# Kernel optimization log

Measured on AMD Instinct MI355X. Metric: run time of the kernel, lower is better.

The kernel has to match this reference:

```python
import jax, jax.numpy as jnp
import numpy as np

N_NODES = 100000
N_EDGES = 1600000
DIMS = [2, 16, 32, 32, 32, 32, 32, 16, 2]


def setup_inputs() -> dict:
    key = jax.random.key(0)
    ks = jax.random.split(key, 20)
    inp = {}
    inp["x"] = jax.random.normal(ks[0], (N_NODES, DIMS[0]), dtype=jnp.float32)
    inp["edge_index"] = jax.random.randint(ks[1], (2, N_EDGES), 0, N_NODES, dtype=jnp.int64)
    for i in range(8):
        fan_in, fan_out = DIMS[i], DIMS[i + 1]
        scale = 1.0 / np.sqrt(fan_in)
        inp[f"W{i+1}"] = jax.random.uniform(ks[2 + i], (fan_in, fan_out), minval=-scale, maxval=scale, dtype=jnp.float32)
        inp[f"b{i+1}"] = jnp.zeros((fan_out,), dtype=jnp.float32)
    return inp


def _gcn_layer(h, W, b, src, dst, norm, n):
    # GCNConv: h' = D^{-1/2} (A+I) D^{-1/2} (h W) + b
    m = (h @ W)[src] * norm[:, None]          # [E+N, d_out] gathered messages
    return jax.ops.segment_sum(m, dst, num_segments=n) + b


def reference(x, edge_index, W1, b1, W2, b2, W3, b3, W4, b4, W5, b5, W6, b6, W7, b7, W8, b8):
    n = x.shape[0]
    x_orig = x[:, :2]
    loops = jnp.arange(n, dtype=edge_index.dtype)
    src = jnp.concatenate([edge_index[0], loops])  # self-loops appended
    dst = jnp.concatenate([edge_index[1], loops])
    deg = jax.ops.segment_sum(jnp.ones(src.shape[0], x.dtype), dst, num_segments=n)
    dinv = jnp.where(deg > 0, jax.lax.rsqrt(deg), 0.0)
    norm = dinv[src] * dinv[dst]               # symmetric normalization per edge
    params = [(W1, b1), (W2, b2), (W3, b3), (W4, b4), (W5, b5), (W6, b6), (W7, b7), (W8, b8)]
    h = x
    for i, (W, b) in enumerate(params):
        h = _gcn_layer(h, W, b, src, dst, norm, n)
        if i < 7:
            h = jax.nn.relu(h)  # dropout is identity in eval mode
    return h + x_orig
```

## Files before the change

kernel.cpp:

```cpp
#include <hip/hip_runtime.h>
#include <hip/hip_fp16.h>

#define NN 100000
#define NE 1600000
#define SCAN_BLK 1024
#define NBLK ((NN + SCAN_BLK - 1) / SCAN_BLK)

#define EB 6144
#define NBE ((NE + EB - 1) / EB)
#define BSH 10
#define NBUCK ((NN + 1023) >> BSH)
#define BCAP 18432


__global__ void k_init(int* __restrict__ bcur) {
    int i = blockIdx.x * blockDim.x + threadIdx.x;
    if (i < NBUCK) bcur[i] = i * BCAP;
}

__global__ __launch_bounds__(256) void k_bucket(
    const int* __restrict__ ei, int* __restrict__ bcur,
    long long* __restrict__ pairs, int nE) {
    __shared__ int cnt[NBUCK];
    __shared__ int sc[NBUCK];
    __shared__ int rc[NBUCK];
    __shared__ int gbase[NBUCK];
    __shared__ int tmp[256];
    __shared__ long long st[EB];

    int base = blockIdx.x * EB;
    int lim = nE - base; if (lim > EB) lim = EB;
    int tid = threadIdx.x;

    for (int i = tid; i < NBUCK; i += 256) cnt[i] = 0;
    __syncthreads();
    for (int i = tid; i < lim; i += 256) {
        int d = ei[nE + base + i];
        atomicAdd(&cnt[d >> BSH], 1);
    }
    __syncthreads();
    {
        int v = (tid < NBUCK) ? cnt[tid] : 0;
        tmp[tid] = v;
        __syncthreads();
        for (int off = 1; off < 256; off <<= 1) {
            int add = (tid >= off) ? tmp[tid - off] : 0;
            __syncthreads();
            tmp[tid] += add;
            __syncthreads();
        }
        if (tid < NBUCK) {
            int e = tmp[tid] - v;
            sc[tid] = e;
            rc[tid] = e;
            gbase[tid] = (v > 0) ? atomicAdd(&bcur[tid], v) : 0;
        }
    }
    __syncthreads();
    for (int i = tid; i < lim; i += 256) {
        int s = ei[base + i];
        int d = ei[nE + base + i];
        int p = atomicAdd(&rc[d >> BSH], 1);
        st[p] = ((long long)d << 32) | (unsigned int)s;
    }
    __syncthreads();
    for (int i = tid; i < lim; i += 256) {
        long long pr = st[i];
        int b = (int)(pr >> 32) >> BSH;
        pairs[gbase[b] + (i - sc[b])] = pr;
    }
}

__global__ __launch_bounds__(256) void k_count2(
    const long long* __restrict__ pairs, const int* __restrict__ bcur,
    int* __restrict__ deg) {
    __shared__ int cnt[1 << BSH];
    int b = blockIdx.x;
    int gb = b * BCAP;
    int m = bcur[b] - gb;
    for (int i = threadIdx.x; i < (1 << BSH); i += 256) cnt[i] = 0;
    __syncthreads();
    for (int i = threadIdx.x; i < m; i += 256) {
        int d = (int)(pairs[gb + i] >> 32);
        atomicAdd(&cnt[d & ((1 << BSH) - 1)], 1);
    }
    __syncthreads();
    int base = b << BSH;
    for (int i = threadIdx.x; i < (1 << BSH); i += 256) {
        int v = base + i;
        if (v < NN) deg[v] = cnt[i];
    }
}

__global__ __launch_bounds__(SCAN_BLK) void k_scan1(
    const int* __restrict__ deg, int* __restrict__ exc, int* __restrict__ bsum, int n) {
    __shared__ int sh[SCAN_BLK];
    int tid = threadIdx.x;
    int i = blockIdx.x * SCAN_BLK + tid;
    int v = (i < n) ? ((deg[i] + 7) & ~7) : 0;
    sh[tid] = v;
    __syncthreads();
    for (int off = 1; off < SCAN_BLK; off <<= 1) {
        int add = (tid >= off) ? sh[tid - off] : 0;
        __syncthreads();
        sh[tid] += add;
        __syncthreads();
    }
    if (i < n) exc[i] = sh[tid] - v;
    if (tid == SCAN_BLK - 1) bsum[blockIdx.x] = sh[tid];
}

__global__ __launch_bounds__(128) void k_scan2(int* __restrict__ bsum, int nb) {
    __shared__ int sh[128];
    int tid = threadIdx.x;
    int v = (tid < nb) ? bsum[tid] : 0;
    sh[tid] = v;
    __syncthreads();
    for (int off = 1; off < 128; off <<= 1) {
        int add = (tid >= off) ? sh[tid - off] : 0;
        __syncthreads();
        sh[tid] += add;
        __syncthreads();
    }
    if (tid < nb) bsum[tid] = sh[tid] - v;
}

__global__ __launch_bounds__(SCAN_BLK) void k_scan3(
    const int* __restrict__ exc, const int* __restrict__ bsum,
    const int* __restrict__ deg, const float* __restrict__ x,
    int* __restrict__ rowptr, float* __restrict__ dinv,
    __half2* __restrict__ hd0, int n) {
    int i = blockIdx.x * SCAN_BLK + threadIdx.x;
    if (i >= n) return;
    int r = exc[i] + bsum[blockIdx.x];
    rowptr[i] = r;
    float dv = rsqrtf((float)(deg[i] + 1));
    dinv[i] = dv;
    hd0[i] = __floats2half2_rn(x[2 * i] * dv, x[2 * i + 1] * dv);
    if (i == n - 1) rowptr[n] = r + ((deg[i] + 7) & ~7);
    if (i == 0) hd0[n] = __floats2half2_rn(0.f, 0.f);
}

__global__ __launch_bounds__(256) void k_fill3(
    const long long* __restrict__ pairs, const int* __restrict__ bcur,
    const int* __restrict__ rowptr, int* __restrict__ csr_src) {
    __shared__ int lcur[1 << BSH];
    int b = blockIdx.x;
    int gb = b * BCAP;
    int m = bcur[b] - gb;
    int base = b << BSH;
    for (int i = threadIdx.x; i < (1 << BSH); i += 256) {
        int v = base + i;
        lcur[i] = (v < NN) ? rowptr[v] : 0;
    }
    __syncthreads();
    for (int i = threadIdx.x; i < m; i += 256) {
        long long pr = pairs[gb + i];
        int d = (int)(pr >> 32);
        int s = (int)(pr & 0xffffffffLL);
        int pos = atomicAdd(&lcur[d & ((1 << BSH) - 1)], 1);
        csr_src[pos] = s;
    }
    __syncthreads();
    for (int i = threadIdx.x; i < (1 << BSH); i += 256) {
        int v = base + i;
        if (v < NN) {
            int e = lcur[i];
            int pe = rowptr[v + 1];
            for (; e < pe; ++e) csr_src[e] = NN;
        }
    }
}


__global__ __launch_bounds__(256) void k_layer1(
    const int* __restrict__ rowptr, const int* __restrict__ csr_src,
    const __half2* __restrict__ hd0, const float* __restrict__ Wg,
    const float* __restrict__ bg, const float* __restrict__ dinv,
    __half* __restrict__ hd1, int n) {
    __shared__ float sW[32];
    if (threadIdx.x < 32) sW[threadIdx.x] = Wg[threadIdx.x];
    __syncthreads();
    int v = blockIdx.x * 16 + threadIdx.x / 16;
    int l = threadIdx.x & 15;
    if (v > n) return;
    if (v == n) { hd1[v * 16 + l] = __float2half(0.f); return; }
    int lo = rowptr[v], hi = rowptr[v + 1];
    float a0 = 0.f, a1 = 0.f;
    for (int j = lo + l; j < hi; j += 16) {
        float2 h = __half22float2(hd0[csr_src[j]]);
        a0 += h.x; a1 += h.y;
    }
#pragma unroll
    for (int off = 8; off >= 1; off >>= 1) {
        a0 += __shfl_xor(a0, off, 16);
        a1 += __shfl_xor(a1, off, 16);
    }
    float dv = dinv[v];
    float2 hs = __half22float2(hd0[v]);
    a0 = (a0 + hs.x) * dv;
    a1 = (a1 + hs.y) * dv;
    float o = bg[l] + a0 * sW[l] + a1 * sW[16 + l];
    hd1[v * 16 + l] = __float2half(fmaxf(o, 0.f) * dv);
}

template <int DIN, int DOUT, bool RELU, bool LAST>
__global__ __launch_bounds__(256) void k_layerU(
    const int* __restrict__ rowptr, const int* __restrict__ csr_src,
    const __half* __restrict__ hd_in, const float* __restrict__ Wg,
    const float* __restrict__ bg, const float* __restrict__ dinv,
    const float* __restrict__ xorig, __half* __restrict__ hout_h,
    float* __restrict__ hout_f, int n) {
    constexpr int PQ = DIN / 2;
    int lane = threadIdx.x & 63;

    int v = blockIdx.x * 4 + (threadIdx.x >> 6);
    if (v > n) return;
    if (v == n) {
        if (!LAST && lane < DOUT) hout_h[(size_t)v * DOUT + lane] = __float2half(0.f);
        return;
    }
    int q = lane & (PQ - 1);
    int lo = rowptr[v], hi = rowptr[v + 1];
    int nch = (hi - lo) >> 3;
    const uint* hp = (const uint*)hd_in;
    float accx = 0.f, accy = 0.f;

    if constexpr (DIN == 32) {
        int el = lane >> 4;
        int b0 = lo + el;
        int sA0 = csr_src[b0 +  0], sB0 = csr_src[b0 +  4];
        int sA1 = csr_src[b0 +  8], sB1 = csr_src[b0 + 12];
        int sA2 = csr_src[b0 + 16], sB2 = csr_src[b0 + 20];
        int sA3 = csr_src[b0 + 24], sB3 = csr_src[b0 + 28];
        if (nch < 1) { sA0 = NN; sB0 = NN; }
        if (nch < 2) { sA1 = NN; sB1 = NN; }
        if (nch < 3) { sA2 = NN; sB2 = NN; }
        if (nch < 4) { sA3 = NN; sB3 = NN; }
        uint uA0 = hp[(size_t)sA0 * 16 + q], uB0 = hp[(size_t)sB0 * 16 + q];
        uint uA1 = hp[(size_t)sA1 * 16 + q], uB1 = hp[(size_t)sB1 * 16 + q];
        uint uA2 = hp[(size_t)sA2 * 16 + q], uB2 = hp[(size_t)sB2 * 16 + q];
        uint uA3 = hp[(size_t)sA3 * 16 + q], uB3 = hp[(size_t)sB3 * 16 + q];
        __half2 h0 = __hadd2(*(const __half2*)&uA0, *(const __half2*)&uB0);
        __half2 h1 = __hadd2(*(const __half2*)&uA1, *(const __half2*)&uB1);
        __half2 h2 = __hadd2(*(const __half2*)&uA2, *(const __half2*)&uB2);
        __half2 h3 = __hadd2(*(const __half2*)&uA3, *(const __half2*)&uB3);
        float2 f0 = __half22float2(h0), f1 = __half22float2(h1);
        float2 f2 = __half22float2(h2), f3 = __half22float2(h3);
        accx = (f0.x + f1.x) + (f2.x + f3.x);
        accy = (f0.y + f1.y) + (f2.y + f3.y);
        for (int j = lo + 32; j < hi; j += 8) {
            int sA = csr_src[j + el], sB = csr_src[j + 4 + el];
            uint uA = hp[(size_t)sA * 16 + q], uB = hp[(size_t)sB * 16 + q];
            __half2 hs = __hadd2(*(const __half2*)&uA, *(const __half2*)&uB);
            float2 f = __half22float2(hs);
            accx += f.x; accy += f.y;
        }
    } else {
        int el = lane >> 3;
        int b0 = lo + el;
        int s0 = csr_src[b0 +  0];
        int s1 = csr_src[b0 +  8];
        int s2 = csr_src[b0 + 16];
        int s3 = csr_src[b0 + 24];
        if (nch < 1) s0 = NN;
        if (nch < 2) s1 = NN;
        if (nch < 3) s2 = NN;
        if (nch < 4) s3 = NN;
        uint u0 = hp[(size_t)s0 * 8 + q];
        uint u1 = hp[(size_t)s1 * 8 + q];
        uint u2 = hp[(size_t)s2 * 8 + q];
        uint u3 = hp[(size_t)s3 * 8 + q];
        __half2 ha = __hadd2(*(const __half2*)&u0, *(const __half2*)&u1);
        __half2 hb = __hadd2(*(const __half2*)&u2, *(const __half2*)&u3);
        float2 fa = __half22float2(ha), fb = __half22float2(hb);
        accx = fa.x + fb.x;
        accy = fa.y + fb.y;
        for (int j = lo + 32; j < hi; j += 8) {
            int s = csr_src[j + el];
            uint u = hp[(size_t)s * 8 + q];
            float2 f = __half22float2(*(const __half2*)&u);
            accx += f.x; accy += f.y;
        }
    }
#pragma unroll
    for (int off = PQ; off < 64; off <<= 1) {
        accx += __shfl_xor(accx, off, 64);
        accy += __shfl_xor(accy, off, 64);
    }
    {
        uint us = hp[(size_t)v * PQ + q];
        float2 fs = __half22float2(*(const __half2*)&us);
        accx += fs.x; accy += fs.y;
    }
    float dv = dinv[v];
    float a0 = accx * dv;
    float a1 = accy * dv;

    if constexpr (DIN == 32) {
        int el2 = lane >> 4;
        int gl = lane & 15;
        int f2b = el2 * 8;
        if constexpr (DOUT == 32) {
            float o0 = 0.f, o1 = 0.f;
#pragma unroll
            for (int k = 0; k < 8; ++k) {
                int f2 = f2b + k;
                float src = (f2 & 1) ? a1 : a0;
                float hf = __shfl(src, f2 >> 1, 16);
                o0 = fmaf(hf, Wg[f2 * 32 + gl], o0);
                o1 = fmaf(hf, Wg[f2 * 32 + gl + 16], o1);
            }
            o0 += __shfl_xor(o0, 16, 64);
            o1 += __shfl_xor(o1, 16, 64);
            o0 += __shfl_xor(o0, 32, 64);
            o1 += __shfl_xor(o1, 32, 64);
            if (lane < 16) {
                float r0 = bg[gl] + o0;
                float r1 = bg[gl + 16] + o1;
                if (RELU) { r0 = fmaxf(r0, 0.f); r1 = fmaxf(r1, 0.f); }
                hout_h[(size_t)v * 32 + gl]      = __float2half(r0 * dv);
                hout_h[(size_t)v * 32 + gl + 16] = __float2half(r1 * dv);
            }
        } else {
            float o0 = 0.f;
#pragma unroll
            for (int k = 0; k < 8; ++k) {
                int f2 = f2b + k;
                float src = (f2 & 1) ? a1 : a0;
                float hf = __shfl(src, f2 >> 1, 16);
                o0 = fmaf(hf, Wg[f2 * 16 + gl], o0);
            }
            o0 += __shfl_xor(o0, 16, 64);
            o0 += __shfl_xor(o0, 32, 64);
            if (lane < 16) {
                float r0 = bg[gl] + o0;
                if (RELU) r0 = fmaxf(r0, 0.f);
                hout_h[(size_t)v * 16 + gl] = __float2half(r0 * dv);
            }
        }
    } else {
        int g = lane & (DOUT - 1);
        float o = bg[g];
#pragma unroll
        for (int f2 = 0; f2 < DIN; ++f2) {
            float src = (f2 & 1) ? a1 : a0;
            float hf = __shfl(src, f2 >> 1, PQ);
            o = fmaf(hf, Wg[f2 * DOUT + g], o);
        }
        if (lane < DOUT) {
            if (LAST) {
                hout_f[(size_t)v * DOUT + g] = o + xorig[(size_t)v * 2 + g];
            } else {
                if (RELU) o = fmaxf(o, 0.f);
                hout_h[(size_t)v * DOUT + g] = __float2half(o * dv);
            }
        }
    }
}


extern "C" void kernel_launch(void* const* d_in, const int* in_sizes, int n_in,
                              void* d_out, int out_size, void* d_ws, size_t ws_size,
                              hipStream_t stream) {
    const float* x = (const float*)d_in[0];
    const int* ei = (const int*)d_in[1];
    const float* W[8];
    const float* B[8];
    for (int i = 0; i < 8; ++i) {
        W[i] = (const float*)d_in[2 + 2 * i];
        B[i] = (const float*)d_in[3 + 2 * i];
    }
    float* out = (float*)d_out;

    char* ws = (char*)d_ws;
    int*       deg     = (int*)      (ws + 0);
    float*     dinv    = (float*)    (ws + 400128);
    int*       rowptr  = (int*)      (ws + 800256);
    int*       exc     = (int*)      (ws + 1200384);
    int*       bsum    = (int*)      (ws + 1600512);
    int*       bcur    = (int*)      (ws + 1601024);
    long long* pairs   = (long long*)(ws + 1601536);
    int*       csr_src = (int*)      (ws + 16052224);
    __half*    hdA     = (__half*)   (ws + 25652224);
    __half*    hdB     = (__half*)   (ws + 32052352);

    dim3 blk(256);

    k_init<<<1, 128, 0, stream>>>(bcur);
    k_bucket<<<NBE, blk, 0, stream>>>(ei, bcur, pairs, NE);
    k_count2<<<NBUCK, blk, 0, stream>>>(pairs, bcur, deg);
    k_scan1<<<NBLK, SCAN_BLK, 0, stream>>>(deg, exc, bsum, NN);
    k_scan2<<<1, 128, 0, stream>>>(bsum, NBLK);
    k_scan3<<<NBLK, SCAN_BLK, 0, stream>>>(exc, bsum, deg, x, rowptr, dinv, (__half2*)hdA, NN);
    k_fill3<<<NBUCK, blk, 0, stream>>>(pairs, bcur, rowptr, csr_src);

    int g1 = (NN + 16) / 16;
    int gS = NN / 4 + 1;
    int gL = (NN + 3) / 4;

    k_layer1<<<g1, blk, 0, stream>>>(rowptr, csr_src, (const __half2*)hdA, W[0], B[0], dinv, hdB, NN);
    k_layerU<16, 32, true, false><<<gS, blk, 0, stream>>>(rowptr, csr_src, hdB, W[1], B[1], dinv, x, hdA, out, NN);
    k_layerU<32, 32, true, false><<<gS, blk, 0, stream>>>(rowptr, csr_src, hdA, W[2], B[2], dinv, x, hdB, out, NN);
    k_layerU<32, 32, true, false><<<gS, blk, 0, stream>>>(rowptr, csr_src, hdB, W[3], B[3], dinv, x, hdA, out, NN);
    k_layerU<32, 32, true, false><<<gS, blk, 0, stream>>>(rowptr, csr_src, hdA, W[4], B[4], dinv, x, hdB, out, NN);
    k_layerU<32, 32, true, false><<<gS, blk, 0, stream>>>(rowptr, csr_src, hdB, W[5], B[5], dinv, x, hdA, out, NN);
    k_layerU<32, 16, true, false><<<gS, blk, 0, stream>>>(rowptr, csr_src, hdA, W[6], B[6], dinv, x, hdB, out, NN);
    k_layerU<16, 2, false, true><<<gL, blk, 0, stream>>>(rowptr, csr_src, hdB, W[7], B[7], dinv, x, hdA, out, NN);
}
```

Baseline: 343.6 us.

## Use wave-per-node layer1 gather, 32-bit indexing, and paired half2 output stores

Layer 1 now assigns a full 64-lane wavefront per node instead of 16 lanes, gathering up to 64 neighbours per iteration with a full-wave shuffle reduction and reading weights directly from global instead of shared memory. All layer kernels drop size_t index casts to use 32-bit address arithmetic. The DIN=32/DOUT=32 path remaps each lane to adjacent output pairs so results are written as one half2 store. The remap changes which weight column each lane reads but stays consistent. Layer 1 now launches four times as many waves, and most lanes sit idle on low-degree nodes (average about 17 neighbours).

```diff
diff --git a/kernel.cpp b/kernel.cpp
--- a/kernel.cpp
+++ b/kernel.cpp
@@ -178,30 +178,41 @@
     const __half2* __restrict__ hd0, const float* __restrict__ Wg,
     const float* __restrict__ bg, const float* __restrict__ dinv,
     __half* __restrict__ hd1, int n) {
-    __shared__ float sW[32];
-    if (threadIdx.x < 32) sW[threadIdx.x] = Wg[threadIdx.x];
-    __syncthreads();
-    int v = blockIdx.x * 16 + threadIdx.x / 16;
-    int l = threadIdx.x & 15;
+    int lane = threadIdx.x & 63;
+    int v = blockIdx.x * 4 + (threadIdx.x >> 6);
     if (v > n) return;
-    if (v == n) { hd1[v * 16 + l] = __float2half(0.f); return; }
+    if (v == n) {
+        if (lane < 16) hd1[v * 16 + lane] = __float2half(0.f);
+        return;
+    }
     int lo = rowptr[v], hi = rowptr[v + 1];
-    float a0 = 0.f, a1 = 0.f;
-    for (int j = lo + l; j < hi; j += 16) {
-        float2 h = __half22float2(hd0[csr_src[j]]);
-        a0 += h.x; a1 += h.y;
+    const uint* hp = (const uint*)hd0;
+    int j = lo + lane;
+    int sc = csr_src[j];
+    int s = (j < hi) ? sc : NN;
+    uint u = hp[s];
+    float2 f = __half22float2(*(const __half2*)&u);
+    float a0 = f.x, a1 = f.y;
+    for (int jb = lo + 64; jb < hi; jb += 64) {
+        int jj = jb + lane;
+        int s2 = (jj < hi) ? csr_src[jj] : NN;
+        uint u2 = hp[s2];
+        float2 f2v = __half22float2(*(const __half2*)&u2);
+        a0 += f2v.x; a1 += f2v.y;
     }
 #pragma unroll
-    for (int off = 8; off >= 1; off >>= 1) {
-        a0 += __shfl_xor(a0, off, 16);
-        a1 += __shfl_xor(a1, off, 16);
+    for (int off = 1; off < 64; off <<= 1) {
+        a0 += __shfl_xor(a0, off, 64);
+        a1 += __shfl_xor(a1, off, 64);
     }
     float dv = dinv[v];
     float2 hs = __half22float2(hd0[v]);
     a0 = (a0 + hs.x) * dv;
     a1 = (a1 + hs.y) * dv;
-    float o = bg[l] + a0 * sW[l] + a1 * sW[16 + l];
-    hd1[v * 16 + l] = __float2half(fmaxf(o, 0.f) * dv);
+    if (lane < 16) {
+        float o = bg[lane] + a0 * Wg[lane] + a1 * Wg[16 + lane];
+        hd1[v * 16 + lane] = __float2half(fmaxf(o, 0.f) * dv);
+    }
 }
 
 template <int DIN, int DOUT, bool RELU, bool LAST>
@@ -217,7 +228,7 @@
     int v = blockIdx.x * 4 + (threadIdx.x >> 6);
     if (v > n) return;
     if (v == n) {
-        if (!LAST && lane < DOUT) hout_h[(size_t)v * DOUT + lane] = __float2half(0.f);
+        if (!LAST && lane < DOUT) hout_h[v * DOUT + lane] = __float2half(0.f);
         return;
     }
     int q = lane & (PQ - 1);
@@ -237,10 +248,10 @@
         if (nch < 2) { sA1 = NN; sB1 = NN; }
         if (nch < 3) { sA2 = NN; sB2 = NN; }
         if (nch < 4) { sA3 = NN; sB3 = NN; }
-        uint uA0 = hp[(size_t)sA0 * 16 + q], uB0 = hp[(size_t)sB0 * 16 + q];
-        uint uA1 = hp[(size_t)sA1 * 16 + q], uB1 = hp[(size_t)sB1 * 16 + q];
-        uint uA2 = hp[(size_t)sA2 * 16 + q], uB2 = hp[(size_t)sB2 * 16 + q];
-        uint uA3 = hp[(size_t)sA3 * 16 + q], uB3 = hp[(size_t)sB3 * 16 + q];
+        uint uA0 = hp[sA0 * 16 + q], uB0 = hp[sB0 * 16 + q];
+        uint uA1 = hp[sA1 * 16 + q], uB1 = hp[sB1 * 16 + q];
+        uint uA2 = hp[sA2 * 16 + q], uB2 = hp[sB2 * 16 + q];
+        uint uA3 = hp[sA3 * 16 + q], uB3 = hp[sB3 * 16 + q];
         __half2 h0 = __hadd2(*(const __half2*)&uA0, *(const __half2*)&uB0);
         __half2 h1 = __hadd2(*(const __half2*)&uA1, *(const __half2*)&uB1);
         __half2 h2 = __hadd2(*(const __half2*)&uA2, *(const __half2*)&uB2);
@@ -251,7 +262,7 @@
         accy = (f0.y + f1.y) + (f2.y + f3.y);
         for (int j = lo + 32; j < hi; j += 8) {
             int sA = csr_src[j + el], sB = csr_src[j + 4 + el];
-            uint uA = hp[(size_t)sA * 16 + q], uB = hp[(size_t)sB * 16 + q];
+            uint uA = hp[sA * 16 + q], uB = hp[sB * 16 + q];
             __half2 hs = __hadd2(*(const __half2*)&uA, *(const __half2*)&uB);
             float2 f = __half22float2(hs);
             accx += f.x; accy += f.y;
@@ -267,10 +278,10 @@
         if (nch < 2) s1 = NN;
         if (nch < 3) s2 = NN;
         if (nch < 4) s3 = NN;
-        uint u0 = hp[(size_t)s0 * 8 + q];
-        uint u1 = hp[(size_t)s1 * 8 + q];
-        uint u2 = hp[(size_t)s2 * 8 + q];
-        uint u3 = hp[(size_t)s3 * 8 + q];
+        uint u0 = hp[s0 * 8 + q];
+        uint u1 = hp[s1 * 8 + q];
+        uint u2 = hp[s2 * 8 + q];
+        uint u3 = hp[s3 * 8 + q];
         __half2 ha = __hadd2(*(const __half2*)&u0, *(const __half2*)&u1);
         __half2 hb = __hadd2(*(const __half2*)&u2, *(const __half2*)&u3);
         float2 fa = __half22float2(ha), fb = __half22float2(hb);
@@ -278,7 +289,7 @@
         accy = fa.y + fb.y;
         for (int j = lo + 32; j < hi; j += 8) {
             int s = csr_src[j + el];
-            uint u = hp[(size_t)s * 8 + q];
+            uint u = hp[s * 8 + q];
             float2 f = __half22float2(*(const __half2*)&u);
             accx += f.x; accy += f.y;
         }
@@ -289,7 +300,7 @@
         accy += __shfl_xor(accy, off, 64);
     }
     {
-        uint us = hp[(size_t)v * PQ + q];
+        uint us = hp[v * PQ + q];
         float2 fs = __half22float2(*(const __half2*)&us);
         accx += fs.x; accy += fs.y;
     }
@@ -308,19 +319,19 @@
                 int f2 = f2b + k;
                 float src = (f2 & 1) ? a1 : a0;
                 float hf = __shfl(src, f2 >> 1, 16);
-                o0 = fmaf(hf, Wg[f2 * 32 + gl], o0);
-                o1 = fmaf(hf, Wg[f2 * 32 + gl + 16], o1);
+                o0 = fmaf(hf, Wg[f2 * 32 + 2 * gl], o0);
+                o1 = fmaf(hf, Wg[f2 * 32 + 2 * gl + 1], o1);
             }
             o0 += __shfl_xor(o0, 16, 64);
             o1 += __shfl_xor(o1, 16, 64);
             o0 += __shfl_xor(o0, 32, 64);
             o1 += __shfl_xor(o1, 32, 64);
             if (lane < 16) {
-                float r0 = bg[gl] + o0;
-                float r1 = bg[gl + 16] + o1;
+                float r0 = bg[2 * gl] + o0;
+                float r1 = bg[2 * gl + 1] + o1;
                 if (RELU) { r0 = fmaxf(r0, 0.f); r1 = fmaxf(r1, 0.f); }
-                hout_h[(size_t)v * 32 + gl]      = __float2half(r0 * dv);
-                hout_h[(size_t)v * 32 + gl + 16] = __float2half(r1 * dv);
+                *reinterpret_cast<__half2*>(&hout_h[v * 32 + 2 * gl]) =
+                    __floats2half2_rn(r0 * dv, r1 * dv);
             }
         } else {
             float o0 = 0.f;
@@ -336,7 +347,7 @@
             if (lane < 16) {
                 float r0 = bg[gl] + o0;
                 if (RELU) r0 = fmaxf(r0, 0.f);
-                hout_h[(size_t)v * 16 + gl] = __float2half(r0 * dv);
+                hout_h[v * 16 + gl] = __float2half(r0 * dv);
             }
         }
     } else {
@@ -350,10 +361,10 @@
         }
         if (lane < DOUT) {
             if (LAST) {
-                hout_f[(size_t)v * DOUT + g] = o + xorig[(size_t)v * 2 + g];
+                hout_f[v * DOUT + g] = o + xorig[v * 2 + g];
             } else {
                 if (RELU) o = fmaxf(o, 0.f);
-                hout_h[(size_t)v * DOUT + g] = __float2half(o * dv);
+                hout_h[v * DOUT + g] = __float2half(o * dv);
             }
         }
     }
@@ -395,11 +406,10 @@
     k_scan3<<<NBLK, SCAN_BLK, 0, stream>>>(exc, bsum, deg, x, rowptr, dinv, (__half2*)hdA, NN);
     k_fill3<<<NBUCK, blk, 0, stream>>>(pairs, bcur, rowptr, csr_src);
 
-    int g1 = (NN + 16) / 16;
     int gS = NN / 4 + 1;
     int gL = (NN + 3) / 4;
 
-    k_layer1<<<g1, blk, 0, stream>>>(rowptr, csr_src, (const __half2*)hdA, W[0], B[0], dinv, hdB, NN);
+    k_layer1<<<gS, blk, 0, stream>>>(rowptr, csr_src, (const __half2*)hdA, W[0], B[0], dinv, hdB, NN);
     k_layerU<16, 32, true, false><<<gS, blk, 0, stream>>>(rowptr, csr_src, hdB, W[1], B[1], dinv, x, hdA, out, NN);
     k_layerU<32, 32, true, false><<<gS, blk, 0, stream>>>(rowptr, csr_src, hdA, W[2], B[2], dinv, x, hdB, out, NN);
     k_layerU<32, 32, true, false><<<gS, blk, 0, stream>>>(rowptr, csr_src, hdB, W[3], B[3], dinv, x, hdA, out, NN);
```

Measured after the change: 385.8 us. 1.12x slower.
